# Kernel tuning notes

Measured on AMD Instinct MI355X. Metric: run time of the kernel, lower is better.

The kernel has to match this reference:

```python
import jax, jax.numpy as jnp
import numpy as np

GENE_NUM = 3000
N_NODES = 50000
N_EDGES = 1000000
DIM = 128


def setup_inputs() -> dict:
    key = jax.random.key(0)
    ks = jax.random.split(key, 8)
    h = jax.random.normal(ks[0], (N_NODES, DIM), dtype=jnp.float32)
    alpha = jax.random.normal(ks[1], (GENE_NUM + 2,), dtype=jnp.float32)
    edge_weight = jax.random.uniform(ks[2], (N_EDGES,), dtype=jnp.float32)
    # Xavier-uniform Linear weight, zero bias
    gain = float(np.sqrt(2.0))  # calculate_gain('relu')
    bound = gain * np.sqrt(6.0 / (DIM + DIM))
    W = jax.random.uniform(ks[3], (DIM, DIM), minval=-bound, maxval=bound, dtype=jnp.float32)
    b = jnp.zeros((DIM,), dtype=jnp.float32)
    # node ids: genes 0..GENE_NUM-1 have id = gene index (>=0); cells have id = -1 (<0)
    node_id = jnp.concatenate([
        jnp.arange(GENE_NUM, dtype=jnp.int64),
        -jnp.ones((N_NODES - GENE_NUM,), dtype=jnp.int64),
    ])
    edge_src = jax.random.randint(ks[4], (N_EDGES,), 0, N_NODES, dtype=jnp.int64)
    edge_dst = jax.random.randint(ks[5], (N_EDGES,), 0, N_NODES, dtype=jnp.int64)
    return {"h": h, "alpha": alpha, "edge_weight": edge_weight, "W": W, "b": b,
            "node_id": node_id, "edge_src": edge_src, "edge_dst": edge_dst}


def reference(h, alpha, edge_weight, W, b, node_id, edge_src, edge_dst):
    gene_num = alpha.shape[0] - 2
    src_id = node_id[edge_src]  # [E]
    dst_id = node_id[edge_dst]  # [E]
    # default: cell self-loop alpha -> index gene_num + 1
    idx = jnp.full(edge_src.shape, gene_num + 1, dtype=jnp.int32)
    idx = jnp.where((src_id >= 0) & (dst_id < 0), src_id.astype(jnp.int32), idx)   # gene->cell: beta[src]
    idx = jnp.where((dst_id >= 0) & (src_id < 0), dst_id.astype(jnp.int32), idx)   # cell->gene: beta[dst]
    idx = jnp.where((dst_id >= 0) & (src_id >= 0), gene_num, idx)                  # gene self-loop alpha
    # gather -> per-edge message [E, D]
    coeff = alpha[idx] * edge_weight                     # [E]
    msg = h[edge_src] * coeff[:, None]                   # [E, D]
    # scatter-mean over destination nodes
    n = h.shape[0]
    summ = jax.ops.segment_sum(msg, edge_dst, num_segments=n)           # [N, D]
    cnt = jax.ops.segment_sum(jnp.ones_like(edge_weight), edge_dst, num_segments=n)
    neigh = summ / jnp.maximum(cnt, 1.0)[:, None]
    # MLP: dropout(eval, identity) -> Linear -> ReLU -> norm(identity)
    z = jax.nn.relu(neigh @ W.T + b)
    return z
```

## Files before the change

### kernel.cpp

```cpp
#include <hip/hip_runtime.h>

#define D 128
#define PSHIFT 6
#define PSIZE 64
#define EDGES_PER_BLK 4096
#define CAP 2048
#define CAPP 2244
#define MAXPART 1024
#define NCHUNK 4

typedef __attribute__((ext_vector_type(8))) short bf16x8;
typedef __attribute__((ext_vector_type(4))) float f32x4;

__device__ __forceinline__ unsigned short f2bf(float f) {
  unsigned int u = __float_as_uint(f);
  u = (u + 0x7fffu + ((u >> 16) & 1)) >> 16;
  return (unsigned short)u;
}

__global__ __launch_bounds__(512) void cvt_hist_kernel(
    const float* __restrict__ h, unsigned short* __restrict__ h16, int total4,
    const int* __restrict__ edst, int* __restrict__ g_hist, int E,
    int cvtBlocks, int N) {
  if ((int)blockIdx.x < cvtBlocks) {
    int i = blockIdx.x * 512 + threadIdx.x;
    if (i >= total4) return;
    float4 v = ((const float4*)h)[i];
    ushort4 o;
    o.x = f2bf(v.x); o.y = f2bf(v.y); o.z = f2bf(v.z); o.w = f2bf(v.w);
    int f = i * 4;
    int n = f >> 7;
    int d = f & 127;
    int c = d >> 5;
    int wi = d & 31;
    ((ushort4*)h16)[(size_t)c * N * 8 + n * 8 + (wi >> 2)] = o;
    return;
  }
  __shared__ int cnt[MAXPART];
  int t = threadIdx.x;
  cnt[t] = 0; cnt[t + 512] = 0;
  __syncthreads();
  int eb = (blockIdx.x - cvtBlocks) * EDGES_PER_BLK;
#pragma unroll
  for (int q = 0; q < 8; ++q) {
    int e = eb + q * 512 + t;
    if (e < E) atomicAdd(&cnt[edst[e] >> PSHIFT], 1);
  }
  __syncthreads();
  int c = cnt[t];
  if (c > 0) atomicAdd(&g_hist[t], c);
  c = cnt[t + 512];
  if (c > 0) atomicAdd(&g_hist[t + 512], c);
}

__global__ __launch_bounds__(512) void part_scan_kernel(
    const int* __restrict__ g_hist, int* __restrict__ part_off,
    int* __restrict__ g_cursor, int E, int npart) {
  __shared__ int ts[512];
  int t = threadIdx.x;
  int i0 = 2 * t, i1 = 2 * t + 1;
  int v0 = (i0 < npart) ? g_hist[i0] : 0;
  int v1 = (i1 < npart) ? g_hist[i1] : 0;
  ts[t] = v0 + v1;
  __syncthreads();
  for (int off = 1; off < 512; off <<= 1) {
    int x = (t >= off) ? ts[t - off] : 0;
    __syncthreads();
    ts[t] += x;
    __syncthreads();
  }
  int excl = ts[t] - (v0 + v1);
  if (i0 < npart) { part_off[i0] = excl; g_cursor[i0] = excl; }
  if (i1 < npart) { part_off[i1] = excl + v0; g_cursor[i1] = excl + v0; }
  if (t == 0) part_off[npart] = E;
}

__global__ __launch_bounds__(512) void bin_scatter_kernel(
    const float* __restrict__ alpha, const float* __restrict__ ew,
    const int* __restrict__ node_id, const int* __restrict__ esrc,
    const int* __restrict__ edst, int* __restrict__ g_cursor,
    int2* __restrict__ recs, int E, int gene_num) {
  __shared__ int2 lrec[EDGES_PER_BLK];
  __shared__ unsigned short lbin[EDGES_PER_BLK];
  __shared__ int cnt[MAXPART], offl[MAXPART], gbase[MAXPART];
  __shared__ int ts[512];

  int t = threadIdx.x;
  cnt[t] = 0; cnt[t + 512] = 0;
  __syncthreads();

  int eb = blockIdx.x * EDGES_PER_BLK;
  int rx[8]; float rc[8]; int rb[8]; int rk[8];
#pragma unroll
  for (int q = 0; q < 8; ++q) {
    int e = eb + q * 512 + t;
    rk[q] = -1;
    if (e < E) {
      int src = esrc[e];
      int dst = edst[e];
      int sid = node_id[src];
      int did = node_id[dst];
      int idx;
      if (sid >= 0) idx = (did >= 0) ? gene_num : sid;
      else          idx = (did >= 0) ? did : (gene_num + 1);
      rc[q] = alpha[idx] * ew[e];
      rx[q] = src | ((dst & (PSIZE - 1)) << 16);
      int b = dst >> PSHIFT;
      rb[q] = b;
      rk[q] = atomicAdd(&cnt[b], 1);
    }
  }
  __syncthreads();

  int c0 = cnt[2 * t], c1 = cnt[2 * t + 1];
  ts[t] = c0 + c1;
  __syncthreads();
  for (int off = 1; off < 512; off <<= 1) {
    int x = (t >= off) ? ts[t - off] : 0;
    __syncthreads();
    ts[t] += x;
    __syncthreads();
  }
  int exclp = ts[t] - (c0 + c1);
  offl[2 * t] = exclp;
  offl[2 * t + 1] = exclp + c0;
  __syncthreads();

#pragma unroll
  for (int q = 0; q < 8; ++q) {
    if (rk[q] >= 0) {
      int ls = offl[rb[q]] + rk[q];
      lrec[ls] = make_int2(rx[q], __float_as_int(rc[q]));
      lbin[ls] = (unsigned short)rb[q];
    }
  }
  __syncthreads();

  {
    int c = cnt[t];
    if (c > 0) gbase[t] = atomicAdd(&g_cursor[t], c);
    c = cnt[t + 512];
    if (c > 0) gbase[t + 512] = atomicAdd(&g_cursor[t + 512], c);
  }
  __syncthreads();

  int tot = E - eb;
  if (tot > EDGES_PER_BLK) tot = EDGES_PER_BLK;
  for (int s = t; s < tot; s += 512) {
    int b = lbin[s];
    recs[gbase[b] + (s - offl[b])] = lrec[s];
  }
}

__global__ __launch_bounds__(512) void sort_kernel(
    int2* __restrict__ recs, const int* __restrict__ part_off,
    int* __restrict__ cnt_g, int* __restrict__ off_g,
    int* __restrict__ pad_g, int* __restrict__ rk_g) {
  __shared__ int2 lrec[CAP];
  __shared__ int cnt[PSIZE], offl[PSIZE], padl[PSIZE];

  int t = threadIdx.x;
  int p = blockIdx.x;
  if (t < PSIZE) cnt[t] = 0;
  __syncthreads();

  int start = part_off[p];
  int R = part_off[p + 1] - start;
  if (R > CAP) R = CAP;

  int2 rq[4]; int dlq[4]; int rkq[4];
#pragma unroll
  for (int q = 0; q < 4; ++q) {
    int s = q * 512 + t;
    rkq[q] = -1;
    if (s < R) {
      int2 r = recs[start + s];
      rq[q] = r;
      int dl = (r.x >> 16) & (PSIZE - 1);
      dlq[q] = dl;
      rkq[q] = atomicAdd(&cnt[dl], 1);
    }
  }
  __syncthreads();

  if (t < PSIZE) { offl[t] = cnt[t]; padl[t] = (cnt[t] + 3) & ~3; }
  __syncthreads();
  for (int off = 1; off < PSIZE; off <<= 1) {
    int x = 0, y = 0;
    if (t < PSIZE && t >= off) { x = offl[t - off]; y = padl[t - off]; }
    __syncthreads();
    if (t < PSIZE) { offl[t] += x; padl[t] += y; }
    __syncthreads();
  }
  if (t < PSIZE) {
    offl[t] -= cnt[t];
    padl[t] -= (cnt[t] + 3) & ~3;
  }
  __syncthreads();

#pragma unroll
  for (int q = 0; q < 4; ++q)
    if (rkq[q] >= 0) lrec[offl[dlq[q]] + rkq[q]] = rq[q];
  __syncthreads();

  for (int s = t; s < R; s += 512) recs[start + s] = lrec[s];
  if (t < PSIZE) {
    cnt_g[p * PSIZE + t] = cnt[t];
    off_g[p * PSIZE + t] = offl[t];
    pad_g[p * PSIZE + t] = padl[t];
    int my = cnt[t];
    int r = 0;
    for (int j = 0; j < PSIZE; ++j) {
      int cj = cnt[j];
      r += (cj > my) || (cj == my && j < t);
    }
    rk_g[p * PSIZE + r] = t;
  }
}

__global__ __launch_bounds__(512) void part_acc_kernel(
    const unsigned short* __restrict__ h16, const int2* __restrict__ recs,
    const int* __restrict__ part_off, const int* __restrict__ cnt_g,
    const int* __restrict__ off_g, const int* __restrict__ pad_g,
    const int* __restrict__ rk_g, float* __restrict__ neigh, int N) {
  __shared__ int2 lrec[CAPP];
  __shared__ int cnt[PSIZE], offl[PSIZE], padl[PSIZE], rkm[PSIZE];

  int t = threadIdx.x;
  int p = blockIdx.x >> 2;
  int chunk = blockIdx.x & 3;

  int start = part_off[p];
  int R = part_off[p + 1] - start;
  if (R > CAP) R = CAP;

  if (t < PSIZE) {
    cnt[t] = cnt_g[p * PSIZE + t];
    offl[t] = off_g[p * PSIZE + t];
    padl[t] = pad_g[p * PSIZE + t];
    rkm[t] = rk_g[p * PSIZE + t];
  }
  {
    int2 z = make_int2(0, 0);
    for (int q = t; q < CAPP; q += 512) lrec[q] = z;
  }
  __syncthreads();

  for (int s = t; s < R; s += 512) {
    int2 r = recs[start + s];
    int dl = (r.x >> 16) & (PSIZE - 1);
    lrec[padl[dl] + (s - offl[dl])] = r;
  }
  __syncthreads();

  int w = t >> 6;
  int l = t & 63;
  int esub = l >> 4;
  int dpair = l & 15;
  const unsigned int* hpc =
      ((const unsigned int*)h16) + (size_t)chunk * N * 16 + dpair;

#pragma unroll
  for (int h2 = 0; h2 < 2; ++h2) {
    int Q = (h2 == 0) ? w : (15 - w);
    int myDl = rkm[Q * 4 + esub];
    int myCnt = cnt[myDl];
    int myOff = padl[myDl];
    int myPad = (myCnt + 3) & ~3;
    float ax = 0.f, ay = 0.f;
    int k = 0;
    for (; k + 8 <= myPad; k += 8) {
      unsigned int v[8]; float c[8];
#pragma unroll
      for (int q = 0; q < 8; ++q) {
        int2 r = lrec[myOff + k + q];
        c[q] = __int_as_float(r.y);
        v[q] = hpc[(size_t)(r.x & 0xffff) * 16];
      }
#pragma unroll
      for (int q = 0; q < 8; ++q) {
        ax += c[q] * __uint_as_float(v[q] << 16);
        ay += c[q] * __uint_as_float(v[q] & 0xffff0000u);
      }
    }
    if (k < myPad) {
      unsigned int v[4]; float c[4];
#pragma unroll
      for (int q = 0; q < 4; ++q) {
        int2 r = lrec[myOff + k + q];
        c[q] = __int_as_float(r.y);
        v[q] = hpc[(size_t)(r.x & 0xffff) * 16];
      }
#pragma unroll
      for (int q = 0; q < 4; ++q) {
        ax += c[q] * __uint_as_float(v[q] << 16);
        ay += c[q] * __uint_as_float(v[q] & 0xffff0000u);
      }
    }
    int dst = p * PSIZE + myDl;
    if (dst < N) {
      float inv = 1.0f / (float)(myCnt > 0 ? myCnt : 1);
      ((float2*)neigh)[(size_t)dst * 64 + chunk * 16 + dpair] =
          make_float2(ax * inv, ay * inv);
    }
  }
}

__global__ __launch_bounds__(256) void mlp_mfma_kernel(
    const float* __restrict__ W, const float* __restrict__ bias,
    float* __restrict__ io, int N) {
  __shared__ __align__(16) unsigned short Wl[128 * 128];

  int t = threadIdx.x;
#pragma unroll
  for (int i = 0; i < 8; ++i) {
    int chunk = t + 256 * i;
    int row = chunk >> 4;
    int cb = chunk & 15;
    const float* gp = W + (size_t)row * 128 + cb * 8;
    float4 a = *(const float4*)gp;
    float4 b = *(const float4*)(gp + 4);
    bf16x8 v;
    v[0] = (short)f2bf(a.x); v[1] = (short)f2bf(a.y);
    v[2] = (short)f2bf(a.z); v[3] = (short)f2bf(a.w);
    v[4] = (short)f2bf(b.x); v[5] = (short)f2bf(b.y);
    v[6] = (short)f2bf(b.z); v[7] = (short)f2bf(b.w);
    *(bf16x8*)((char*)Wl + row * 256 + ((cb ^ (row & 7)) << 4)) = v;
  }
  __syncthreads();

  int l = t & 63;
  int w = t >> 6;
  int kg = l >> 4;
  int m_base = blockIdx.x * 64 + w * 16;
  int arow = m_base + (l & 15);
  if (arow >= N) arow = N - 1;

  bf16x8 af[4];
  const float* ap = io + (size_t)arow * 128 + kg * 8;
#pragma unroll
  for (int kk = 0; kk < 4; ++kk) {
    float4 a = *(const float4*)(ap + kk * 32);
    float4 b = *(const float4*)(ap + kk * 32 + 4);
    bf16x8 v;
    v[0] = (short)f2bf(a.x); v[1] = (short)f2bf(a.y);
    v[2] = (short)f2bf(a.z); v[3] = (short)f2bf(a.w);
    v[4] = (short)f2bf(b.x); v[5] = (short)f2bf(b.y);
    v[6] = (short)f2bf(b.z); v[7] = (short)f2bf(b.w);
    af[kk] = v;
  }

#pragma unroll
  for (int c = 0; c < 8; ++c) {
    f32x4 acc = {0.f, 0.f, 0.f, 0.f};
    int row_w = c * 16 + (l & 15);
    int rs = row_w & 7;
#pragma unroll
    for (int kk = 0; kk < 4; ++kk) {
      int cb = kk * 4 + kg;
      bf16x8 bf = *(bf16x8*)((char*)Wl + row_w * 256 + ((cb ^ rs) << 4));
      acc = __builtin_amdgcn_mfma_f32_16x16x32_bf16(af[kk], bf, acc, 0, 0, 0);
    }
    int j = c * 16 + (l & 15);
    float bj = bias[j];
#pragma unroll
    for (int r = 0; r < 4; ++r) {
      int m = m_base + kg * 4 + r;
      if (m < N) io[(size_t)m * 128 + j] = fmaxf(acc[r] + bj, 0.0f);
    }
  }
}

extern "C" void kernel_launch(void* const* d_in, const int* in_sizes, int n_in,
                              void* d_out, int out_size, void* d_ws, size_t ws_size,
                              hipStream_t stream) {
  const float* h     = (const float*)d_in[0];
  const float* alpha = (const float*)d_in[1];
  const float* ew    = (const float*)d_in[2];
  const float* W     = (const float*)d_in[3];
  const float* bias  = (const float*)d_in[4];
  const int* node_id = (const int*)d_in[5];
  const int* esrc    = (const int*)d_in[6];
  const int* edst    = (const int*)d_in[7];
  float* out = (float*)d_out;

  int E = in_sizes[2];
  int N = in_sizes[5];
  int gene_num = in_sizes[1] - 2;
  int npart = (N + PSIZE - 1) / PSIZE;
  int eblocks = (E + EDGES_PER_BLK - 1) / EDGES_PER_BLK;
  int total4 = N * D / 4;
  int cvtBlocks = (total4 + 511) / 512;

  int* g_hist   = (int*)d_ws;
  int* part_off = g_hist + MAXPART;
  int* g_cursor = part_off + MAXPART + 1;
  int* cnt_g    = g_cursor + MAXPART;
  int* off_g    = cnt_g + MAXPART * PSIZE;
  int* pad_g    = off_g + MAXPART * PSIZE;
  int* rk_g     = pad_g + MAXPART * PSIZE;
  size_t h16_off = ((size_t)(3 * MAXPART + 1 + 4 * MAXPART * PSIZE) * sizeof(int)
                    + 15) & ~(size_t)15;
  unsigned short* h16 = (unsigned short*)((char*)d_ws + h16_off);
  size_t rec_off = (h16_off + (size_t)N * D * sizeof(unsigned short) + 15) & ~(size_t)15;
  int2* recs = (int2*)((char*)d_ws + rec_off);
  size_t need = rec_off + (size_t)E * sizeof(int2);
  if (ws_size < need) return;

  hipMemsetAsync(g_hist, 0, MAXPART * sizeof(int), stream);

  cvt_hist_kernel<<<cvtBlocks + eblocks, 512, 0, stream>>>(
      h, h16, total4, edst, g_hist, E, cvtBlocks, N);
  part_scan_kernel<<<1, 512, 0, stream>>>(g_hist, part_off, g_cursor, E, npart);
  bin_scatter_kernel<<<eblocks, 512, 0, stream>>>(alpha, ew, node_id, esrc,
                                                  edst, g_cursor, recs, E,
                                                  gene_num);
  sort_kernel<<<npart, 512, 0, stream>>>(recs, part_off, cnt_g, off_g, pad_g,
                                         rk_g);
  part_acc_kernel<<<npart * NCHUNK, 512, 0, stream>>>(h16, recs, part_off,
                                                      cnt_g, off_g, pad_g,
                                                      rk_g, out, N);
  {
    int blocks = (N + 63) / 64;
    mlp_mfma_kernel<<<blocks, 256, 0, stream>>>(W, bias, out, N);
  }
}
```

Before: 108.4 us.

## Read sorted edge records directly from global memory in accumulation kernel

The accumulation kernel no longer stages each partition's records into padded shared memory. It reads the sorted records straight from global memory using per-destination offsets, with a masked tail instead of padding to multiples of four. This removes the padded-offset scan, the pad array, the LDS zeroing and staging pass and two block barriers. In exchange, every record is fetched from global or L2 once per chunk block (four times total), the tail may read up to eight entries past the end, and LDS occupancy limits go away.

After: 122.5 us. 13.0% more time.

```diff
diff --git a/kernel.cpp b/kernel.cpp
--- a/kernel.cpp
+++ b/kernel.cpp
@@ -5,7 +5,6 @@
 #define PSIZE 64
 #define EDGES_PER_BLK 4096
 #define CAP 2048
-#define CAPP 2244
 #define MAXPART 1024
 #define NCHUNK 4
 
@@ -155,9 +154,9 @@
 __global__ __launch_bounds__(512) void sort_kernel(
     int2* __restrict__ recs, const int* __restrict__ part_off,
     int* __restrict__ cnt_g, int* __restrict__ off_g,
-    int* __restrict__ pad_g, int* __restrict__ rk_g) {
+    int* __restrict__ rk_g) {
   __shared__ int2 lrec[CAP];
-  __shared__ int cnt[PSIZE], offl[PSIZE], padl[PSIZE];
+  __shared__ int cnt[PSIZE], offl[PSIZE];
 
   int t = threadIdx.x;
   int p = blockIdx.x;
@@ -183,19 +182,16 @@
   }
   __syncthreads();
 
-  if (t < PSIZE) { offl[t] = cnt[t]; padl[t] = (cnt[t] + 3) & ~3; }
+  if (t < PSIZE) offl[t] = cnt[t];
   __syncthreads();
   for (int off = 1; off < PSIZE; off <<= 1) {
-    int x = 0, y = 0;
-    if (t < PSIZE && t >= off) { x = offl[t - off]; y = padl[t - off]; }
-    __syncthreads();
-    if (t < PSIZE) { offl[t] += x; padl[t] += y; }
-    __syncthreads();
-  }
-  if (t < PSIZE) {
-    offl[t] -= cnt[t];
-    padl[t] -= (cnt[t] + 3) & ~3;
-  }
+    int x = 0;
+    if (t < PSIZE && t >= off) x = offl[t - off];
+    __syncthreads();
+    if (t < PSIZE) offl[t] += x;
+    __syncthreads();
+  }
+  if (t < PSIZE) offl[t] -= cnt[t];
   __syncthreads();
 
 #pragma unroll
@@ -207,7 +203,6 @@
   if (t < PSIZE) {
     cnt_g[p * PSIZE + t] = cnt[t];
     off_g[p * PSIZE + t] = offl[t];
-    pad_g[p * PSIZE + t] = padl[t];
     int my = cnt[t];
     int r = 0;
     for (int j = 0; j < PSIZE; ++j) {
@@ -221,37 +216,12 @@
 __global__ __launch_bounds__(512) void part_acc_kernel(
     const unsigned short* __restrict__ h16, const int2* __restrict__ recs,
     const int* __restrict__ part_off, const int* __restrict__ cnt_g,
-    const int* __restrict__ off_g, const int* __restrict__ pad_g,
-    const int* __restrict__ rk_g, float* __restrict__ neigh, int N) {
-  __shared__ int2 lrec[CAPP];
-  __shared__ int cnt[PSIZE], offl[PSIZE], padl[PSIZE], rkm[PSIZE];
-
+    const int* __restrict__ off_g, const int* __restrict__ rk_g,
+    float* __restrict__ neigh, int N) {
   int t = threadIdx.x;
   int p = blockIdx.x >> 2;
   int chunk = blockIdx.x & 3;
-
   int start = part_off[p];
-  int R = part_off[p + 1] - start;
-  if (R > CAP) R = CAP;
-
-  if (t < PSIZE) {
-    cnt[t] = cnt_g[p * PSIZE + t];
-    offl[t] = off_g[p * PSIZE + t];
-    padl[t] = pad_g[p * PSIZE + t];
-    rkm[t] = rk_g[p * PSIZE + t];
-  }
-  {
-    int2 z = make_int2(0, 0);
-    for (int q = t; q < CAPP; q += 512) lrec[q] = z;
-  }
-  __syncthreads();
-
-  for (int s = t; s < R; s += 512) {
-    int2 r = recs[start + s];
-    int dl = (r.x >> 16) & (PSIZE - 1);
-    lrec[padl[dl] + (s - offl[dl])] = r;
-  }
-  __syncthreads();
 
   int w = t >> 6;
   int l = t & 63;
@@ -263,17 +233,16 @@
 #pragma unroll
   for (int h2 = 0; h2 < 2; ++h2) {
     int Q = (h2 == 0) ? w : (15 - w);
-    int myDl = rkm[Q * 4 + esub];
-    int myCnt = cnt[myDl];
-    int myOff = padl[myDl];
-    int myPad = (myCnt + 3) & ~3;
+    int myDl = rk_g[p * PSIZE + Q * 4 + esub];
+    int myCnt = cnt_g[p * PSIZE + myDl];
+    int myBase = start + off_g[p * PSIZE + myDl];
     float ax = 0.f, ay = 0.f;
     int k = 0;
-    for (; k + 8 <= myPad; k += 8) {
+    for (; k + 8 <= myCnt; k += 8) {
       unsigned int v[8]; float c[8];
 #pragma unroll
       for (int q = 0; q < 8; ++q) {
-        int2 r = lrec[myOff + k + q];
+        int2 r = recs[myBase + k + q];
         c[q] = __int_as_float(r.y);
         v[q] = hpc[(size_t)(r.x & 0xffff) * 16];
       }
@@ -283,13 +252,16 @@
         ay += c[q] * __uint_as_float(v[q] & 0xffff0000u);
       }
     }
-    if (k < myPad) {
+    for (; k < myCnt; k += 4) {
       unsigned int v[4]; float c[4];
 #pragma unroll
       for (int q = 0; q < 4; ++q) {
-        int2 r = lrec[myOff + k + q];
-        c[q] = __int_as_float(r.y);
-        v[q] = hpc[(size_t)(r.x & 0xffff) * 16];
+        int sl = k + q;
+        int2 r = recs[myBase + sl];
+        bool ok = sl < myCnt;
+        c[q] = ok ? __int_as_float(r.y) : 0.f;
+        unsigned int a = ok ? (unsigned int)(r.x & 0xffff) : 0u;
+        v[q] = hpc[(size_t)a * 16];
       }
 #pragma unroll
       for (int q = 0; q < 4; ++q) {
@@ -397,14 +369,13 @@
   int* g_cursor = part_off + MAXPART + 1;
   int* cnt_g    = g_cursor + MAXPART;
   int* off_g    = cnt_g + MAXPART * PSIZE;
-  int* pad_g    = off_g + MAXPART * PSIZE;
-  int* rk_g     = pad_g + MAXPART * PSIZE;
-  size_t h16_off = ((size_t)(3 * MAXPART + 1 + 4 * MAXPART * PSIZE) * sizeof(int)
+  int* rk_g     = off_g + MAXPART * PSIZE;
+  size_t h16_off = ((size_t)(3 * MAXPART + 1 + 3 * MAXPART * PSIZE) * sizeof(int)
                     + 15) & ~(size_t)15;
   unsigned short* h16 = (unsigned short*)((char*)d_ws + h16_off);
   size_t rec_off = (h16_off + (size_t)N * D * sizeof(unsigned short) + 15) & ~(size_t)15;
   int2* recs = (int2*)((char*)d_ws + rec_off);
-  size_t need = rec_off + (size_t)E * sizeof(int2);
+  size_t need = rec_off + (size_t)(E + 8) * sizeof(int2);
   if (ws_size < need) return;
 
   hipMemsetAsync(g_hist, 0, MAXPART * sizeof(int), stream);
@@ -415,11 +386,10 @@
   bin_scatter_kernel<<<eblocks, 512, 0, stream>>>(alpha, ew, node_id, esrc,
                                                   edst, g_cursor, recs, E,
                                                   gene_num);
-  sort_kernel<<<npart, 512, 0, stream>>>(recs, part_off, cnt_g, off_g, pad_g,
-                                         rk_g);
+  sort_kernel<<<npart, 512, 0, stream>>>(recs, part_off, cnt_g, off_g, rk_g);
   part_acc_kernel<<<npart * NCHUNK, 512, 0, stream>>>(h16, recs, part_off,
-                                                      cnt_g, off_g, pad_g,
-                                                      rk_g, out, N);
+                                                      cnt_g, off_g, rk_g,
+                                                      out, N);
   {
     int blocks = (N + 63) / 64;
     mlp_mfma_kernel<<<blocks, 256, 0, stream>>>(W, bias, out, N);
```
